# Performance work log

Hardware: AMD Instinct MI355X
Metric: run time of the kernel (lower is better)

Reference implementation:

```python
import jax, jax.numpy as jnp
import numpy as np
from jax import lax

B, T, D = 16384, 60, 36   # n_traj, n_tp, n_dims
L, C, S = 10, 20, 9       # latent_dim, cluster_num, n_static
OUT = 8                   # mlp out (use_static=False)


def setup_inputs() -> dict:
    key = jax.random.key(0)
    ks = jax.random.split(key, 12)

    def w(k, shape):
        return jax.random.normal(k, shape, jnp.float32) / np.float32(np.sqrt(shape[0]))

    return {
        "data": jax.random.normal(ks[0], (B, T, D), jnp.float32),
        "time_steps": jnp.arange(T, dtype=jnp.float32),
        "static_data": jax.random.normal(ks[1], (B, S), jnp.float32),
        # GRU_unit_cluster gates: Linear(latent_dim + input_dim -> latent_dim)
        "W_update": w(ks[2], (L + D, L)), "b_update": jnp.zeros((L,), jnp.float32),
        "W_reset": w(ks[3], (L + D, L)), "b_reset": jnp.zeros((L,), jnp.float32),
        "W_new": w(ks[4], (L + D, L)), "b_new": jnp.zeros((L,), jnp.float32),
        # infer_emitter_z: Linear(latent_dim + cluster_num -> cluster_num)
        "W_emit": w(ks[5], (L + C, C)), "b_emit": jnp.zeros((C,), jnp.float32),
        # stand-in ODE func (z0_diffeq_solver.ode_func): tanh(Linear(latent->latent))
        "W_ode": w(ks[6], (L, L)), "b_ode": jnp.zeros((L,), jnp.float32),
        # final mlp: Linear(ts*10 + static -> 8)
        "W_mlp": w(ks[7], (T * L + S, OUT)), "b_mlp": jnp.zeros((OUT,), jnp.float32),
    }


def _forward(data, time_steps, static_data,
             W_update, b_update, W_reset, b_reset, W_new, b_new,
             W_emit, b_emit, W_ode, b_ode, W_mlp, b_mlp):
    n_traj = data.shape[0]
    # per-step dt: first step uses the synthetic 0.01 offset, then consecutive diffs
    dts = jnp.concatenate([jnp.full((1,), 0.01, time_steps.dtype), jnp.diff(time_steps)])
    xs = jnp.swapaxes(data, 0, 1)  # [T, B, D]

    def step(carry, inp):
        y_state, y_prob = carry        # [B, L], [B, C]
        x_t, dt = inp                  # [B, D], scalar
        # Euler step of the ODE between observations
        yi_ode = y_state + jnp.tanh(y_state @ W_ode + b_ode) * dt
        # GRU_unit_cluster update
        yc = jnp.concatenate([yi_ode, x_t], axis=-1)          # [B, L+D]
        u = jax.nn.sigmoid(yc @ W_update + b_update)
        r = jax.nn.sigmoid(yc @ W_reset + b_reset)
        cc = jnp.concatenate([yi_ode * r, x_t], axis=-1)
        new = cc @ W_new + b_new
        y_new = (1.0 - u) * new + u * yi_ode                  # [B, L]
        # emit_probs (concat_data=True path)
        zin = jnp.concatenate([y_prob, y_new], axis=-1)       # [B, C+L]
        y_prob_new = jax.nn.softmax(zin @ W_emit + b_emit, axis=-1)
        return (y_new, y_prob_new), y_new

    init = (jnp.zeros((n_traj, L), data.dtype), jnp.zeros((n_traj, C), data.dtype))
    _, states = lax.scan(step, init, (xs, dts))               # states: [T, B, L]

    vec = jnp.swapaxes(states, 0, 1).reshape(n_traj, T * L)   # [B, T*L]
    vec = jnp.concatenate([vec, static_data], axis=-1)        # [B, T*L + S]
    return vec @ W_mlp + b_mlp                                # [B, 8]


def reference(data, time_steps, static_data,
              W_update, b_update, W_reset, b_reset, W_new, b_new,
              W_emit, b_emit, W_ode, b_ode, W_mlp, b_mlp):
    return _forward(data, time_steps, static_data,
                    W_update, b_update, W_reset, b_reset, W_new, b_new,
                    W_emit, b_emit, W_ode, b_ode, W_mlp, b_mlp)
```

## Files before the change

kernel.cpp:

```cpp
#include <hip/hip_runtime.h>
#include <hip/hip_fp16.h>
#include <math.h>

#define B_TRAJ 16384
#define T_STEPS 60
#define D_IN 36
#define L_DIM 10
#define C_NUM 20
#define S_STAT 9
#define OUT_DIM 8
#define TT 2
#define NTILE (T_STEPS / TT)

__device__ __forceinline__ float rcp_fast(float x) { return __builtin_amdgcn_rcpf(x); }
__device__ __forceinline__ float sigm_fast(float x) { return rcp_fast(1.0f + __expf(-x)); }
__device__ __forceinline__ float tanh_fast(float x) {
    x = fminf(fmaxf(x, -10.0f), 10.0f);
    float e = __expf(2.0f * x);
    return (e - 1.0f) * rcp_fast(e + 1.0f);
}
#define WFENCE() __builtin_amdgcn_wave_barrier()

__global__ __launch_bounds__(256) __attribute__((amdgpu_waves_per_eu(4, 8)))
void dgm2_v5(
    const float* __restrict__ data,
    const float* __restrict__ time_steps,
    const float* __restrict__ static_data,
    const float* __restrict__ W_update,
    const float* __restrict__ b_update,
    const float* __restrict__ W_reset,
    const float* __restrict__ b_reset,
    const float* __restrict__ W_new,
    const float* __restrict__ b_new,
    const float* __restrict__ W_emit,
    const float* __restrict__ b_emit,
    const float* __restrict__ W_ode,
    const float* __restrict__ b_ode,
    const float* __restrict__ W_mlp,
    const float* __restrict__ b_mlp,
    float* __restrict__ out)
{
    __shared__ __align__(16) __half xprojH[8][61][32];
    __shared__ __align__(16) float WGX[D_IN][32];
    __shared__ __align__(16) float wbuf[4][292];
    __shared__ float dts[T_STEPS];

    const int tid  = threadIdx.x;
    const int w    = tid >> 6;
    const int lane = tid & 63;
    const int half = lane >> 5;
    const int s    = lane & 31;
    const int ltraj = w * 2 + half;
    const int traj  = blockIdx.x * 8 + ltraj;

    for (int i = tid; i < D_IN * 30; i += 256) {
        const int k = i / 30, c = i % 30;
        float v;
        if (c < 10)      v = W_update[(L_DIM + k) * L_DIM + c];
        else if (c < 20) v = W_reset [(L_DIM + k) * L_DIM + (c - 10)];
        else             v = W_new   [(L_DIM + k) * L_DIM + (c - 20)];
        WGX[k][c] = v;
    }
    for (int i = tid; i < D_IN * 2; i += 256) WGX[i >> 1][30 + (i & 1)] = 0.0f;
    if (tid < T_STEPS) dts[tid] = (tid == 0) ? 0.01f : time_steps[tid] - time_steps[tid - 1];
    __syncthreads();

    {
        float wxp[D_IN];
#pragma unroll
        for (int k = 0; k < D_IN; ++k) wxp[k] = WGX[k][s];

        float* xst = &wbuf[w][0];
        const float* tbase = data + (size_t)(blockIdx.x * 8 + w * 2) * (T_STEPS * D_IN);
        const int sh  = lane / 18;
        const int sr  = lane % 18;
        const int stt = sr / 9;
        const int sc  = sr % 9;
        const bool stg = (lane < 36);

        if (stg) {
            const float4 v = *reinterpret_cast<const float4*>(
                tbase + (size_t)sh * (T_STEPS * D_IN) + stt * D_IN + sc * 4);
            *reinterpret_cast<float4*>(xst + ((0 * 2 + sh) * TT + stt) * 36 + sc * 4) = v;
        }
        WFENCE();

        for (int tile = 0; tile < NTILE; ++tile) {
            const int cb = tile & 1, nb = cb ^ 1;
            float4 pf = make_float4(0.f, 0.f, 0.f, 0.f);
            if (stg && (tile + 1 < NTILE)) {
                pf = *reinterpret_cast<const float4*>(
                    tbase + (size_t)sh * (T_STEPS * D_IN) + ((tile + 1) * TT + stt) * D_IN + sc * 4);
            }
#pragma unroll
            for (int tt = 0; tt < TT; ++tt) {
                const float* xrow = xst + ((cb * 2 + half) * TT + tt) * 36;
                float acc = 0.0f;
#pragma unroll
                for (int c = 0; c < 9; ++c) {
                    const float4 x4 = *reinterpret_cast<const float4*>(xrow + c * 4);
                    acc += x4.x * wxp[c * 4]     + x4.y * wxp[c * 4 + 1]
                         + x4.z * wxp[c * 4 + 2] + x4.w * wxp[c * 4 + 3];
                }
                if (s < 30) xprojH[ltraj][tile * TT + tt][s] = __float2half(acc);
            }
            if (stg && (tile + 1 < NTILE)) {
                *reinterpret_cast<float4*>(xst + ((nb * 2 + sh) * TT + stt) * 36 + sc * 4) = pf;
            }
            WFENCE();
        }
    }

    const bool uo = (s < 10);
    const bool ro = (s >= 10 && s < 20);
    const bool no = (s >= 20 && s < 30);
    const bool eo = (s >= 10 && s < 30);
    const int  gcol = uo ? s : (ro ? (s - 10) : (no ? (s - 20) : 0));

    const float* Wg = uo ? W_update : (ro ? W_reset : W_new);
    float wgy[L_DIM];
#pragma unroll
    for (int k = 0; k < L_DIM; ++k) wgy[k] = (s < 30) ? Wg[k * L_DIM + gcol] : 0.0f;

    float waux[30];
#pragma unroll
    for (int k = 0; k < 30; ++k) {
        float v = 0.0f;
        if (eo) v = W_emit[k * C_NUM + (s - 10)];
        else if (uo && k < L_DIM) v = W_ode[k * L_DIM + s];
        waux[k] = v;
    }
    const float bg    = uo ? b_update[s] : (ro ? b_reset[gcol] : (no ? b_new[gcol] : 0.0f));
    const float bode  = uo ? b_ode[s] : 0.0f;
    const float bemit = eo ? b_emit[s - 10] : 0.0f;

    float* bcYI = &wbuf[w][0]  + half * 12;
    float* bcR  = &wbuf[w][24] + half * 12;
    float* bcN  = &wbuf[w][48] + half * 12;
    float* bcY  = &wbuf[w][72] + half * 12;
    float* bcP  = &wbuf[w][96] + half * 20;

    float y[L_DIM];
#pragma unroll
    for (int k = 0; k < L_DIM; ++k) y[k] = 0.0f;
    float yown = 0.0f;
    if (eo) bcP[s - 10] = 0.0f;
    WFENCE();

    for (int t = 0; t < T_STEPS; ++t) {
        const float dt = dts[t];

        float g = bode;
#pragma unroll
        for (int k = 0; k < L_DIM; ++k) g += y[k] * waux[k];
        const float yis = fmaf(tanh_fast(g), dt, yown);
        if (uo) bcYI[s] = yis;
        WFENCE();
        {
            const float4 a = *reinterpret_cast<const float4*>(bcYI);
            const float4 b = *reinterpret_cast<const float4*>(bcYI + 4);
            const float2 c = *reinterpret_cast<const float2*>(bcYI + 8);
            y[0] = a.x; y[1] = a.y; y[2] = a.z; y[3] = a.w;
            y[4] = b.x; y[5] = b.y; y[6] = b.z; y[7] = b.w;
            y[8] = c.x; y[9] = c.y;
        }

        const float xa = __half2float(xprojH[ltraj][t][s]);
        const float accB = bg + xa;
        float accY = 0.0f;
#pragma unroll
        for (int k = 0; k < L_DIM; ++k) accY += y[k] * wgy[k];
        const float uval = sigm_fast(accB + accY);
        if (ro) bcR[s - 10] = uval;
        WFENCE();

        float accN = accB;
        {
            const float4 a = *reinterpret_cast<const float4*>(bcR);
            const float4 b = *reinterpret_cast<const float4*>(bcR + 4);
            const float2 c = *reinterpret_cast<const float2*>(bcR + 8);
            const float rv[L_DIM] = {a.x, a.y, a.z, a.w, b.x, b.y, b.z, b.w, c.x, c.y};
#pragma unroll
            for (int k = 0; k < L_DIM; ++k) accN += (y[k] * rv[k]) * wgy[k];
        }
        if (no) bcN[s - 20] = accN;
        WFENCE();

        if (uo) {
            const float nv = bcN[s];
            const float yn = fmaf(uval, yis - nv, nv);
            yown = yn;
            bcY[s] = yn;
            xprojH[ltraj][t][s] = __float2half(yn);
        }
        WFENCE();
        {
            const float4 a = *reinterpret_cast<const float4*>(bcY);
            const float4 b = *reinterpret_cast<const float4*>(bcY + 4);
            const float2 c = *reinterpret_cast<const float2*>(bcY + 8);
            y[0] = a.x; y[1] = a.y; y[2] = a.z; y[3] = a.w;
            y[4] = b.x; y[5] = b.y; y[6] = b.z; y[7] = b.w;
            y[8] = c.x; y[9] = c.y;
        }

        float zdot = 0.0f, zsum = 0.0f;
#pragma unroll
        for (int q = 0; q < 5; ++q) {
            const float4 z4 = *reinterpret_cast<const float4*>(bcP + q * 4);
            zdot += z4.x * waux[q * 4]     + z4.y * waux[q * 4 + 1]
                  + z4.z * waux[q * 4 + 2] + z4.w * waux[q * 4 + 3];
            zsum += (z4.x + z4.y) + (z4.z + z4.w);
        }
        const float pinv = (t == 0) ? 0.0f : rcp_fast(zsum);
        float ev = fmaf(zdot, pinv, bemit);
#pragma unroll
        for (int k = 0; k < L_DIM; ++k) ev += y[k] * waux[20 + k];
        const float zv = __expf(fminf(ev, 60.0f));
        if (eo) bcP[s - 10] = zv;
        WFENCE();
    }

    WFENCE();
    {
        const int g = s >> 3, col = s & 7;
        float o8 = 0.0f;
        for (int tb = 0; tb < 15; ++tb) {
            const int t = g + tb * 4;
            const __half2* yh = reinterpret_cast<const __half2*>(&xprojH[ltraj][t][0]);
            const float* wrow = W_mlp + (size_t)t * L_DIM * OUT_DIM + col;
#pragma unroll
            for (int q = 0; q < 5; ++q) {
                const float2 yv = __half22float2(yh[q]);
                o8 += yv.x * wrow[(2 * q) * OUT_DIM] + yv.y * wrow[(2 * q + 1) * OUT_DIM];
            }
        }
        o8 += __shfl_xor(o8, 8, 32);
        o8 += __shfl_xor(o8, 16, 32);
        if (s < OUT_DIM) {
            const float* stp = static_data + (size_t)traj * S_STAT;
            const float* wms = W_mlp + (size_t)(T_STEPS * L_DIM) * OUT_DIM;
#pragma unroll
            for (int i = 0; i < S_STAT; ++i) o8 += stp[i] * wms[i * OUT_DIM + s];
            out[(size_t)traj * OUT_DIM + s] = o8 + b_mlp[s];
        }
    }
}

extern "C" void kernel_launch(void* const* d_in, const int* in_sizes, int n_in,
                              void* d_out, int out_size, void* d_ws, size_t ws_size,
                              hipStream_t stream) {
    const float* data        = (const float*)d_in[0];
    const float* time_steps  = (const float*)d_in[1];
    const float* static_data = (const float*)d_in[2];
    const float* W_update    = (const float*)d_in[3];
    const float* b_update    = (const float*)d_in[4];
    const float* W_reset     = (const float*)d_in[5];
    const float* b_reset     = (const float*)d_in[6];
    const float* W_new       = (const float*)d_in[7];
    const float* b_new       = (const float*)d_in[8];
    const float* W_emit      = (const float*)d_in[9];
    const float* b_emit      = (const float*)d_in[10];
    const float* W_ode       = (const float*)d_in[11];
    const float* b_ode       = (const float*)d_in[12];
    const float* W_mlp       = (const float*)d_in[13];
    const float* b_mlp       = (const float*)d_in[14];
    float* out = (float*)d_out;

    dim3 grid(B_TRAJ / 8), block(256);
    hipLaunchKernelGGL(dgm2_v5, grid, block, 0, stream,
                       data, time_steps, static_data,
                       W_update, b_update, W_reset, b_reset, W_new, b_new,
                       W_emit, b_emit, W_ode, b_ode, W_mlp, b_mlp, out);
}
```

Before: 343.5 us.

## Pack emission probs in fp16 with dot2, merge ODE/emit dot, drop LDS staging

```diff
diff --git a/kernel.cpp b/kernel.cpp
--- a/kernel.cpp
+++ b/kernel.cpp
@@ -9,8 +9,8 @@
 #define C_NUM 20
 #define S_STAT 9
 #define OUT_DIM 8
-#define TT 2
-#define NTILE (T_STEPS / TT)
+
+typedef __attribute__((ext_vector_type(2))) _Float16 h2;
 
 __device__ __forceinline__ float rcp_fast(float x) { return __builtin_amdgcn_rcpf(x); }
 __device__ __forceinline__ float sigm_fast(float x) { return rcp_fast(1.0f + __expf(-x)); }
@@ -19,10 +19,18 @@
     float e = __expf(2.0f * x);
     return (e - 1.0f) * rcp_fast(e + 1.0f);
 }
+__device__ __forceinline__ h2 f_as_h2(float f) { union { float f; h2 h; } u; u.f = f; return u.h; }
+__device__ __forceinline__ float dot2(h2 a, h2 b, float c) {
+#if __has_builtin(__builtin_amdgcn_fdot2)
+    return __builtin_amdgcn_fdot2(a, b, c, false);
+#else
+    return c + (float)a.x * (float)b.x + (float)a.y * (float)b.y;
+#endif
+}
 #define WFENCE() __builtin_amdgcn_wave_barrier()
 
-__global__ __launch_bounds__(256) __attribute__((amdgpu_waves_per_eu(4, 8)))
-void dgm2_v5(
+__global__ __launch_bounds__(256) __attribute__((amdgpu_waves_per_eu(5, 8)))
+void dgm2_v6(
     const float* __restrict__ data,
     const float* __restrict__ time_steps,
     const float* __restrict__ static_data,
@@ -40,10 +48,9 @@
     const float* __restrict__ b_mlp,
     float* __restrict__ out)
 {
-    __shared__ __align__(16) __half xprojH[8][61][32];
-    __shared__ __align__(16) float WGX[D_IN][32];
-    __shared__ __align__(16) float wbuf[4][292];
-    __shared__ float dts[T_STEPS];
+    __shared__ __align__(16) __half xprojH[8][61][30];
+    __shared__ __align__(16) float wbuf[4][2][64];
+    __shared__ float dts[64];
 
     const int tid  = threadIdx.x;
     const int w    = tid >> 6;
@@ -53,107 +60,87 @@
     const int ltraj = w * 2 + half;
     const int traj  = blockIdx.x * 8 + ltraj;
 
-    for (int i = tid; i < D_IN * 30; i += 256) {
-        const int k = i / 30, c = i % 30;
-        float v;
-        if (c < 10)      v = W_update[(L_DIM + k) * L_DIM + c];
-        else if (c < 20) v = W_reset [(L_DIM + k) * L_DIM + (c - 10)];
-        else             v = W_new   [(L_DIM + k) * L_DIM + (c - 20)];
-        WGX[k][c] = v;
-    }
-    for (int i = tid; i < D_IN * 2; i += 256) WGX[i >> 1][30 + (i & 1)] = 0.0f;
     if (tid < T_STEPS) dts[tid] = (tid == 0) ? 0.01f : time_steps[tid] - time_steps[tid - 1];
     __syncthreads();
 
     {
+        const float* Wsrc = (s < 10) ? W_update : ((s < 20) ? W_reset : W_new);
+        const int cc = (s < 30) ? (s % 10) : 0;
         float wxp[D_IN];
 #pragma unroll
-        for (int k = 0; k < D_IN; ++k) wxp[k] = WGX[k][s];
-
-        float* xst = &wbuf[w][0];
-        const float* tbase = data + (size_t)(blockIdx.x * 8 + w * 2) * (T_STEPS * D_IN);
-        const int sh  = lane / 18;
-        const int sr  = lane % 18;
-        const int stt = sr / 9;
-        const int sc  = sr % 9;
-        const bool stg = (lane < 36);
-
-        if (stg) {
-            const float4 v = *reinterpret_cast<const float4*>(
-                tbase + (size_t)sh * (T_STEPS * D_IN) + stt * D_IN + sc * 4);
-            *reinterpret_cast<float4*>(xst + ((0 * 2 + sh) * TT + stt) * 36 + sc * 4) = v;
-        }
-        WFENCE();
-
-        for (int tile = 0; tile < NTILE; ++tile) {
-            const int cb = tile & 1, nb = cb ^ 1;
-            float4 pf = make_float4(0.f, 0.f, 0.f, 0.f);
-            if (stg && (tile + 1 < NTILE)) {
-                pf = *reinterpret_cast<const float4*>(
-                    tbase + (size_t)sh * (T_STEPS * D_IN) + ((tile + 1) * TT + stt) * D_IN + sc * 4);
+        for (int k = 0; k < D_IN; ++k) wxp[k] = Wsrc[(L_DIM + k) * L_DIM + cc];
+
+        const float* xb = data + (size_t)traj * (T_STEPS * D_IN);
+        for (int t = 0; t < T_STEPS; ++t) {
+            const float* xt = xb + t * D_IN;
+            float acc = 0.0f;
+#pragma unroll
+            for (int g3 = 0; g3 < 3; ++g3) {
+                const float4 a = *reinterpret_cast<const float4*>(xt + g3 * 12);
+                const float4 b = *reinterpret_cast<const float4*>(xt + g3 * 12 + 4);
+                const float4 c = *reinterpret_cast<const float4*>(xt + g3 * 12 + 8);
+                const int k0 = g3 * 12;
+                acc += a.x * wxp[k0 + 0] + a.y * wxp[k0 + 1] + a.z * wxp[k0 + 2] + a.w * wxp[k0 + 3]
+                     + b.x * wxp[k0 + 4] + b.y * wxp[k0 + 5] + b.z * wxp[k0 + 6] + b.w * wxp[k0 + 7]
+                     + c.x * wxp[k0 + 8] + c.y * wxp[k0 + 9] + c.z * wxp[k0 +10] + c.w * wxp[k0 +11];
             }
-#pragma unroll
-            for (int tt = 0; tt < TT; ++tt) {
-                const float* xrow = xst + ((cb * 2 + half) * TT + tt) * 36;
-                float acc = 0.0f;
-#pragma unroll
-                for (int c = 0; c < 9; ++c) {
-                    const float4 x4 = *reinterpret_cast<const float4*>(xrow + c * 4);
-                    acc += x4.x * wxp[c * 4]     + x4.y * wxp[c * 4 + 1]
-                         + x4.z * wxp[c * 4 + 2] + x4.w * wxp[c * 4 + 3];
-                }
-                if (s < 30) xprojH[ltraj][tile * TT + tt][s] = __float2half(acc);
-            }
-            if (stg && (tile + 1 < NTILE)) {
-                *reinterpret_cast<float4*>(xst + ((nb * 2 + sh) * TT + stt) * 36 + sc * 4) = pf;
-            }
-            WFENCE();
-        }
-    }
+            if (s < 30) xprojH[ltraj][t][s] = __float2half(acc);
+        }
+    }
+    WFENCE();
 
     const bool uo = (s < 10);
     const bool ro = (s >= 10 && s < 20);
     const bool no = (s >= 20 && s < 30);
     const bool eo = (s >= 10 && s < 30);
     const int  gcol = uo ? s : (ro ? (s - 10) : (no ? (s - 20) : 0));
+    const int  ecol = s - 10;
 
     const float* Wg = uo ? W_update : (ro ? W_reset : W_new);
     float wgy[L_DIM];
 #pragma unroll
     for (int k = 0; k < L_DIM; ++k) wgy[k] = (s < 30) ? Wg[k * L_DIM + gcol] : 0.0f;
 
-    float waux[30];
-#pragma unroll
-    for (int k = 0; k < 30; ++k) {
+    float wA[L_DIM];
+#pragma unroll
+    for (int k = 0; k < L_DIM; ++k) {
         float v = 0.0f;
-        if (eo) v = W_emit[k * C_NUM + (s - 10)];
-        else if (uo && k < L_DIM) v = W_ode[k * L_DIM + s];
-        waux[k] = v;
+        if (uo) v = W_ode[k * L_DIM + s];
+        else if (eo) v = W_emit[(C_NUM + k) * C_NUM + ecol];
+        wA[k] = v;
+    }
+    h2 wB[10];
+#pragma unroll
+    for (int q = 0; q < 10; ++q) {
+        h2 v; v.x = (_Float16)0.0f; v.y = (_Float16)0.0f;
+        if (eo) {
+            v.x = (_Float16)W_emit[(2 * q) * C_NUM + ecol];
+            v.y = (_Float16)W_emit[(2 * q + 1) * C_NUM + ecol];
+        }
+        wB[q] = v;
     }
     const float bg    = uo ? b_update[s] : (ro ? b_reset[gcol] : (no ? b_new[gcol] : 0.0f));
     const float bode  = uo ? b_ode[s] : 0.0f;
-    const float bemit = eo ? b_emit[s - 10] : 0.0f;
-
-    float* bcYI = &wbuf[w][0]  + half * 12;
-    float* bcR  = &wbuf[w][24] + half * 12;
-    float* bcN  = &wbuf[w][48] + half * 12;
-    float* bcY  = &wbuf[w][72] + half * 12;
-    float* bcP  = &wbuf[w][96] + half * 20;
+    const float bemit = eo ? b_emit[ecol] : 0.0f;
+
+    float*  bcYI = &wbuf[w][half][0];
+    float*  bcR  = &wbuf[w][half][12];
+    float*  bcN  = &wbuf[w][half][24];
+    float*  bcY  = &wbuf[w][half][36];
+    __half* bcPH = reinterpret_cast<__half*>(&wbuf[w][half][48]);
 
     float y[L_DIM];
 #pragma unroll
     for (int k = 0; k < L_DIM; ++k) y[k] = 0.0f;
     float yown = 0.0f;
-    if (eo) bcP[s - 10] = 0.0f;
+    float dotA = 0.0f;
+    if (eo) bcPH[ecol] = __float2half(0.0f);
     WFENCE();
 
     for (int t = 0; t < T_STEPS; ++t) {
         const float dt = dts[t];
 
-        float g = bode;
-#pragma unroll
-        for (int k = 0; k < L_DIM; ++k) g += y[k] * waux[k];
-        const float yis = fmaf(tanh_fast(g), dt, yown);
+        const float yis = fmaf(tanh_fast(bode + dotA), dt, yown);
         if (uo) bcYI[s] = yis;
         WFENCE();
         {
@@ -165,7 +152,7 @@
             y[8] = c.x; y[9] = c.y;
         }
 
-        const float xa = __half2float(xprojH[ltraj][t][s]);
+        const float xa = (s < 30) ? __half2float(xprojH[ltraj][t][s]) : 0.0f;
         const float accB = bg + xa;
         float accY = 0.0f;
 #pragma unroll
@@ -174,16 +161,16 @@
         if (ro) bcR[s - 10] = uval;
         WFENCE();
 
-        float accN = accB;
-        {
+        if (no) {
             const float4 a = *reinterpret_cast<const float4*>(bcR);
             const float4 b = *reinterpret_cast<const float4*>(bcR + 4);
             const float2 c = *reinterpret_cast<const float2*>(bcR + 8);
             const float rv[L_DIM] = {a.x, a.y, a.z, a.w, b.x, b.y, b.z, b.w, c.x, c.y};
+            float accN = accB;
 #pragma unroll
             for (int k = 0; k < L_DIM; ++k) accN += (y[k] * rv[k]) * wgy[k];
-        }
-        if (no) bcN[s - 20] = accN;
+            bcN[s - 20] = accN;
+        }
         WFENCE();
 
         if (uo) {
@@ -203,24 +190,32 @@
             y[8] = c.x; y[9] = c.y;
         }
 
+        float dA = 0.0f;
+#pragma unroll
+        for (int k = 0; k < L_DIM; ++k) dA += y[k] * wA[k];
+        dotA = dA;
+
+        const float4 za = *reinterpret_cast<const float4*>(bcPH);
+        const float4 zb = *reinterpret_cast<const float4*>(bcPH + 8);
+        const float2 zc = *reinterpret_cast<const float2*>(bcPH + 16);
+        h2 zp[10];
+        zp[0] = f_as_h2(za.x); zp[1] = f_as_h2(za.y); zp[2] = f_as_h2(za.z); zp[3] = f_as_h2(za.w);
+        zp[4] = f_as_h2(zb.x); zp[5] = f_as_h2(zb.y); zp[6] = f_as_h2(zb.z); zp[7] = f_as_h2(zb.w);
+        zp[8] = f_as_h2(zc.x); zp[9] = f_as_h2(zc.y);
+        h2 one2; one2.x = (_Float16)1.0f; one2.y = (_Float16)1.0f;
         float zdot = 0.0f, zsum = 0.0f;
 #pragma unroll
-        for (int q = 0; q < 5; ++q) {
-            const float4 z4 = *reinterpret_cast<const float4*>(bcP + q * 4);
-            zdot += z4.x * waux[q * 4]     + z4.y * waux[q * 4 + 1]
-                  + z4.z * waux[q * 4 + 2] + z4.w * waux[q * 4 + 3];
-            zsum += (z4.x + z4.y) + (z4.z + z4.w);
+        for (int q = 0; q < 10; ++q) {
+            zdot = dot2(zp[q], wB[q], zdot);
+            zsum = dot2(zp[q], one2, zsum);
         }
         const float pinv = (t == 0) ? 0.0f : rcp_fast(zsum);
-        float ev = fmaf(zdot, pinv, bemit);
-#pragma unroll
-        for (int k = 0; k < L_DIM; ++k) ev += y[k] * waux[20 + k];
-        const float zv = __expf(fminf(ev, 60.0f));
-        if (eo) bcP[s - 10] = zv;
-        WFENCE();
-    }
-
-    WFENCE();
+        const float ev = fmaf(zdot, pinv, bemit) + dA;
+        const float zv = __expf(fminf(ev, 11.0f));
+        if (eo) bcPH[ecol] = __float2half(zv);
+        WFENCE();
+    }
+
     {
         const int g = s >> 3, col = s & 7;
         float o8 = 0.0f;
@@ -267,7 +262,7 @@
     float* out = (float*)d_out;
 
     dim3 grid(B_TRAJ / 8), block(256);
-    hipLaunchKernelGGL(dgm2_v5, grid, block, 0, stream,
+    hipLaunchKernelGGL(dgm2_v6, grid, block, 0, stream,
                        data, time_steps, static_data,
                        W_update, b_update, W_reset, b_reset, W_new, b_new,
                        W_emit, b_emit, W_ode, b_ode, W_mlp, b_mlp, out);
```

Result: slower. 476.2 us (+38.6%).
